# Kernel tuning notes

Measured on AMD Instinct MI355X. Metric: run time of the kernel, lower is better.

The kernel has to match this reference:

```python
import jax, jax.numpy as jnp
import numpy as np

EPS = 1e-8  # torch.nn.CosineSimilarity default eps


def setup_inputs() -> dict:
    key = jax.random.key(0)
    mapping = jax.random.normal(key, (8192, 512), dtype=jnp.float32)
    return {"mapping": mapping}


def reference(mapping) -> jnp.ndarray:
    # Pairwise cosine distance: 1 - (x_i . x_j) / max(||x_i||*||x_j||, eps)
    # Efficient form: single N x D GEMM + outer product of norms
    dots = mapping @ mapping.T                      # [N, N]
    norms = jnp.linalg.norm(mapping, axis=-1)       # [N]
    denom = jnp.maximum(norms[:, None] * norms[None, :], EPS)
    return 1.0 - dots / denom
```

## Files before the change

kernel.cpp:

```cpp
#include <hip/hip_runtime.h>

typedef __attribute__((ext_vector_type(8))) short bf16x8;
typedef __attribute__((ext_vector_type(8))) unsigned short u16x8;
typedef __attribute__((ext_vector_type(4))) float f32x4;

__device__ __forceinline__ unsigned short f2bf(float f) {
    unsigned int u = __float_as_uint(f);
    u += 0x7fffu + ((u >> 16) & 1u);
    return (unsigned short)(u >> 16);
}

__global__ __launch_bounds__(256) void normalize_rows(
    const float* __restrict__ X, unsigned short* __restrict__ Y) {
    const int wave = threadIdx.x >> 6;
    const int lane = threadIdx.x & 63;
    const long row = (long)blockIdx.x * 4 + wave;

    const float4* xr = (const float4*)(X + row * 512);
    float4 a = xr[lane * 2];
    float4 b = xr[lane * 2 + 1];

    float s = a.x * a.x + a.y * a.y + a.z * a.z + a.w * a.w
            + b.x * b.x + b.y * b.y + b.z * b.z + b.w * b.w;
#pragma unroll
    for (int off = 32; off; off >>= 1) s += __shfl_xor(s, off, 64);

    const float inv = rsqrtf(s);

    u16x8 o;
    o[0] = f2bf(a.x * inv); o[1] = f2bf(a.y * inv);
    o[2] = f2bf(a.z * inv); o[3] = f2bf(a.w * inv);
    o[4] = f2bf(b.x * inv); o[5] = f2bf(b.y * inv);
    o[6] = f2bf(b.z * inv); o[7] = f2bf(b.w * inv);
    ((u16x8*)(Y + row * 512))[lane] = o;
}

#define GLDS16(g, l)                                                         \
    __builtin_amdgcn_global_load_lds(                                        \
        (const __attribute__((address_space(1))) void*)(g),                  \
        (__attribute__((address_space(3))) void*)(l), 16, 0, 0)

#define RD(base, r, c) \
    (*(const bf16x8*)((base) + (r) * 64 + ((((c) ^ ((r) & 7))) << 3)))

__global__ __launch_bounds__(512, 2) void cosdist_gemm_sym(
    const unsigned short* __restrict__ Y, float* __restrict__ out) {
    constexpr int N = 8192, K = 512, BM = 256;
    constexpr int NT = N / BM;
    constexpr int A2 = 2 * NT + 1;
    constexpr int TILE = BM * 64;

    __shared__ __align__(16) short As[2 * TILE];
    __shared__ __align__(16) short Bs[2 * TILE];

    constexpr int NWG = NT * (NT + 1) / 2;
    constexpr int CPX = NWG / 8;
    const int hw = blockIdx.x;
    const int p = (hw & 7) * CPX + (hw >> 3);

    int bi = (int)floorf(((float)A2 - sqrtf((float)(A2 * A2) - 8.0f * (float)p)) * 0.5f);
    while ((bi + 1) * (A2 - (bi + 1)) / 2 <= p) ++bi;
    while (bi * (A2 - bi) / 2 > p) --bi;
    const int bj = bi + (p - bi * (A2 - bi) / 2);
    const int bm = bi * BM, bn = bj * BM;

    const int tid  = threadIdx.x;
    const int lane = tid & 63;
    const int wave = tid >> 6;
    const int wr = wave >> 2;
    const int wc = wave & 3;
    const int frow = lane & 15;
    const int fch  = lane >> 4;

    const int srow = tid >> 3;
    const int sgc  = (tid & 7) ^ (srow & 7);
    const unsigned short* Abase = Y + (size_t)(bm + srow) * K + (sgc << 3);
    const unsigned short* Bbase = Y + (size_t)(bn + srow) * K + (sgc << 3);
    const size_t QSTEP = (size_t)64 * K;

    f32x4 acc[8][4] = {};

#pragma unroll
    for (int j = 0; j < 4; ++j) {
        GLDS16(Abase + (size_t)j * QSTEP, As + j * 4096 + tid * 8);
        GLDS16(Bbase + (size_t)j * QSTEP, Bs + j * 4096 + tid * 8);
    }
    __syncthreads();

    for (int kt = 0; kt < 8; ++kt) {
        const short* Ac = As + (kt & 1) * TILE;
        const short* Bc = Bs + (kt & 1) * TILE;
        short* An = As + ((kt + 1) & 1) * TILE;
        short* Bn = Bs + ((kt + 1) & 1) * TILE;
        const int kn = (kt + 1) << 6;
        const bool pf = (kt < 7);

        bf16x8 af[4][2], bfv[2][2];

        if (pf) {
            GLDS16(Abase + kn, An + tid * 8);
            GLDS16(Bbase + kn, Bn + tid * 8);
        }
#pragma unroll
        for (int m = 0; m < 4; ++m) {
            const int r = wr * 128 + m * 16 + frow;
            af[m][0] = RD(Ac, r, fch);
            af[m][1] = RD(Ac, r, 4 + fch);
        }
#pragma unroll
        for (int n = 0; n < 2; ++n) {
            const int r = wc * 64 + n * 16 + frow;
            bfv[n][0] = RD(Bc, r, fch);
            bfv[n][1] = RD(Bc, r, 4 + fch);
        }
        __builtin_amdgcn_s_setprio(1);
#pragma unroll
        for (int m = 0; m < 4; ++m)
#pragma unroll
            for (int n = 0; n < 2; ++n)
#pragma unroll
                for (int kk = 0; kk < 2; ++kk)
                    acc[m][n] = __builtin_amdgcn_mfma_f32_16x16x32_bf16(
                        af[m][kk], bfv[n][kk], acc[m][n], 0, 0, 0);
        __builtin_amdgcn_s_setprio(0);
        __builtin_amdgcn_s_barrier();

        if (pf) {
            GLDS16(Abase + kn + QSTEP, An + 4096 + tid * 8);
            GLDS16(Bbase + kn + QSTEP, Bn + 4096 + tid * 8);
        }
#pragma unroll
        for (int n = 0; n < 2; ++n) {
            const int r = wc * 64 + (n + 2) * 16 + frow;
            bfv[n][0] = RD(Bc, r, fch);
            bfv[n][1] = RD(Bc, r, 4 + fch);
        }
        __builtin_amdgcn_s_setprio(1);
#pragma unroll
        for (int m = 0; m < 4; ++m)
#pragma unroll
            for (int n = 0; n < 2; ++n)
#pragma unroll
                for (int kk = 0; kk < 2; ++kk)
                    acc[m][n + 2] = __builtin_amdgcn_mfma_f32_16x16x32_bf16(
                        af[m][kk], bfv[n][kk], acc[m][n + 2], 0, 0, 0);
        __builtin_amdgcn_s_setprio(0);
        __builtin_amdgcn_s_barrier();

        if (pf) {
            GLDS16(Abase + kn + 2 * QSTEP, An + 2 * 4096 + tid * 8);
            GLDS16(Bbase + kn + 2 * QSTEP, Bn + 2 * 4096 + tid * 8);
        }
#pragma unroll
        for (int m = 0; m < 4; ++m) {
            const int r = wr * 128 + (m + 4) * 16 + frow;
            af[m][0] = RD(Ac, r, fch);
            af[m][1] = RD(Ac, r, 4 + fch);
        }
        __builtin_amdgcn_s_setprio(1);
#pragma unroll
        for (int m = 0; m < 4; ++m)
#pragma unroll
            for (int n = 0; n < 2; ++n)
#pragma unroll
                for (int kk = 0; kk < 2; ++kk)
                    acc[m + 4][n + 2] = __builtin_amdgcn_mfma_f32_16x16x32_bf16(
                        af[m][kk], bfv[n][kk], acc[m + 4][n + 2], 0, 0, 0);
        __builtin_amdgcn_s_setprio(0);
        __builtin_amdgcn_s_barrier();

        if (pf) {
            GLDS16(Abase + kn + 3 * QSTEP, An + 3 * 4096 + tid * 8);
            GLDS16(Bbase + kn + 3 * QSTEP, Bn + 3 * 4096 + tid * 8);
        }
#pragma unroll
        for (int n = 0; n < 2; ++n) {
            const int r = wc * 64 + n * 16 + frow;
            bfv[n][0] = RD(Bc, r, fch);
            bfv[n][1] = RD(Bc, r, 4 + fch);
        }
        __builtin_amdgcn_s_setprio(1);
#pragma unroll
        for (int m = 0; m < 4; ++m)
#pragma unroll
            for (int n = 0; n < 2; ++n)
#pragma unroll
                for (int kk = 0; kk < 2; ++kk)
                    acc[m + 4][n] = __builtin_amdgcn_mfma_f32_16x16x32_bf16(
                        af[m][kk], bfv[n][kk], acc[m + 4][n], 0, 0, 0);
        __builtin_amdgcn_s_setprio(0);
        __syncthreads();
    }

    const int rbase = bm + wr * 128 + (fch << 2);
    const int cbase = bn + wc * 64 + frow;
    const bool offdiag = (bm != bn);

#pragma unroll
    for (int m = 0; m < 8; ++m)
#pragma unroll
        for (int n = 0; n < 4; ++n) {
            f32x4 v;
#pragma unroll
            for (int r = 0; r < 4; ++r) v[r] = 1.0f - acc[m][n][r];
            const int row = rbase + m * 16;
            const int col = cbase + n * 16;

            *(f32x4*)&out[(size_t)col * N + row] = v;

            if (offdiag) {
#pragma unroll
                for (int r = 0; r < 4; ++r)
                    out[(size_t)(row + r) * N + col] = v[r];
            }
        }
}

extern "C" void kernel_launch(void* const* d_in, const int* in_sizes, int n_in,
                              void* d_out, int out_size, void* d_ws, size_t ws_size,
                              hipStream_t stream) {
    const float* X = (const float*)d_in[0];
    float* out = (float*)d_out;
    unsigned short* Y = (unsigned short*)d_ws;

    const int D = 512;
    const int N = in_sizes[0] / D;

    normalize_rows<<<N / 4, 256, 0, stream>>>(X, Y);

    const int nt = N / 256;
    const int ntiles = nt * (nt + 1) / 2;
    cosdist_gemm_sym<<<ntiles, 512, 0, stream>>>(Y, out);
}
```

Baseline: 372.4 us.

## Reorder tile loads by consumption order and use fine-grained vmcnt waits

Reorders the global-to-LDS load slices of A and B so that the quarter needed first by each phase arrives first. It regroups B rows into 32-row halves per 64-row block to match the per-phase fragment reads. The full __syncthreads at the end of each k-step is replaced with partial s_waitcnt vmcnt plus barriers, so the next tile's loads can stay in flight while compute continues. This aims to cut the stall on whole-tile completion. It relies on precise vmcnt counting and barrier placement, which risks LDS races if any count is wrong.

```diff
diff --git a/kernel.cpp b/kernel.cpp
--- a/kernel.cpp
+++ b/kernel.cpp
@@ -72,20 +72,23 @@
     const int frow = lane & 15;
     const int fch  = lane >> 4;
 
-    const int srow = tid >> 3;
-    const int sgc  = (tid & 7) ^ (srow & 7);
-    const unsigned short* Abase = Y + (size_t)(bm + srow) * K + (sgc << 3);
-    const unsigned short* Bbase = Y + (size_t)(bn + srow) * K + (sgc << 3);
-    const size_t QSTEP = (size_t)64 * K;
+    const int i6  = tid >> 3;
+    const int sgc = (tid & 7) ^ (i6 & 7);
+    const unsigned short* Asrc = Y + (size_t)(bm + i6) * K + (sgc << 3);
+    const int rB = ((i6 >> 5) << 6) + (i6 & 31);
+    const unsigned short* Bsrc = Y + (size_t)(bn + rB) * K + (sgc << 3);
+    const int boff = ((i6 >> 5) << 12) + ((i6 & 31) << 6) + ((tid & 7) << 3);
 
     f32x4 acc[8][4] = {};
 
-#pragma unroll
-    for (int j = 0; j < 4; ++j) {
-        GLDS16(Abase + (size_t)j * QSTEP, As + j * 4096 + tid * 8);
-        GLDS16(Bbase + (size_t)j * QSTEP, Bs + j * 4096 + tid * 8);
-    }
-    __syncthreads();
+    GLDS16(Asrc,                   As + tid * 8);
+    GLDS16(Asrc + 2 * 32768,       As + 2 * 4096 + tid * 8);
+    GLDS16(Asrc + 1 * 32768,       As + 1 * 4096 + tid * 8);
+    GLDS16(Asrc + 3 * 32768,       As + 3 * 4096 + tid * 8);
+    GLDS16(Bsrc,                   Bs + boff);
+    GLDS16(Bsrc + 65536,           Bs + 8192 + boff);
+    GLDS16(Bsrc + 16384,           Bs + 2048 + boff);
+    GLDS16(Bsrc + 81920,           Bs + 10240 + boff);
 
     for (int kt = 0; kt < 8; ++kt) {
         const short* Ac = As + (kt & 1) * TILE;
@@ -97,9 +100,11 @@
 
         bf16x8 af[4][2], bfv[2][2];
 
-        if (pf) {
-            GLDS16(Abase + kn, An + tid * 8);
-            GLDS16(Bbase + kn, Bn + tid * 8);
+        asm volatile("s_waitcnt vmcnt(2)" ::: "memory");
+        __builtin_amdgcn_s_barrier();
+        if (pf) {
+            GLDS16(Asrc + kn,             An + tid * 8);
+            GLDS16(Asrc + 2 * 32768 + kn, An + 2 * 4096 + tid * 8);
         }
 #pragma unroll
         for (int m = 0; m < 4; ++m) {
@@ -123,15 +128,17 @@
                     acc[m][n] = __builtin_amdgcn_mfma_f32_16x16x32_bf16(
                         af[m][kk], bfv[n][kk], acc[m][n], 0, 0, 0);
         __builtin_amdgcn_s_setprio(0);
-        __builtin_amdgcn_s_barrier();
-
-        if (pf) {
-            GLDS16(Abase + kn + QSTEP, An + 4096 + tid * 8);
-            GLDS16(Bbase + kn + QSTEP, Bn + 4096 + tid * 8);
+
+        if (pf) asm volatile("s_waitcnt vmcnt(2)" ::: "memory");
+        else    asm volatile("s_waitcnt vmcnt(0)" ::: "memory");
+        __builtin_amdgcn_s_barrier();
+        if (pf) {
+            GLDS16(Asrc + 1 * 32768 + kn, An + 1 * 4096 + tid * 8);
+            GLDS16(Asrc + 3 * 32768 + kn, An + 3 * 4096 + tid * 8);
         }
 #pragma unroll
         for (int n = 0; n < 2; ++n) {
-            const int r = wc * 64 + (n + 2) * 16 + frow;
+            const int r = wc * 64 + 32 + n * 16 + frow;
             bfv[n][0] = RD(Bc, r, fch);
             bfv[n][1] = RD(Bc, r, 4 + fch);
         }
@@ -145,15 +152,15 @@
                     acc[m][n + 2] = __builtin_amdgcn_mfma_f32_16x16x32_bf16(
                         af[m][kk], bfv[n][kk], acc[m][n + 2], 0, 0, 0);
         __builtin_amdgcn_s_setprio(0);
-        __builtin_amdgcn_s_barrier();
-
-        if (pf) {
-            GLDS16(Abase + kn + 2 * QSTEP, An + 2 * 4096 + tid * 8);
-            GLDS16(Bbase + kn + 2 * QSTEP, Bn + 2 * 4096 + tid * 8);
+
+        __builtin_amdgcn_s_barrier();
+        if (pf) {
+            GLDS16(Bsrc + kn,         Bn + boff);
+            GLDS16(Bsrc + 65536 + kn, Bn + 8192 + boff);
         }
 #pragma unroll
         for (int m = 0; m < 4; ++m) {
-            const int r = wr * 128 + (m + 4) * 16 + frow;
+            const int r = wr * 128 + 64 + m * 16 + frow;
             af[m][0] = RD(Ac, r, fch);
             af[m][1] = RD(Ac, r, 4 + fch);
         }
@@ -167,11 +174,11 @@
                     acc[m + 4][n + 2] = __builtin_amdgcn_mfma_f32_16x16x32_bf16(
                         af[m][kk], bfv[n][kk], acc[m + 4][n + 2], 0, 0, 0);
         __builtin_amdgcn_s_setprio(0);
-        __builtin_amdgcn_s_barrier();
-
-        if (pf) {
-            GLDS16(Abase + kn + 3 * QSTEP, An + 3 * 4096 + tid * 8);
-            GLDS16(Bbase + kn + 3 * QSTEP, Bn + 3 * 4096 + tid * 8);
+
+        __builtin_amdgcn_s_barrier();
+        if (pf) {
+            GLDS16(Bsrc + 16384 + kn, Bn + 2048 + boff);
+            GLDS16(Bsrc + 81920 + kn, Bn + 10240 + boff);
         }
 #pragma unroll
         for (int n = 0; n < 2; ++n) {
@@ -189,7 +196,6 @@
                     acc[m + 4][n] = __builtin_amdgcn_mfma_f32_16x16x32_bf16(
                         af[m][kk], bfv[n][kk], acc[m + 4][n], 0, 0, 0);
         __builtin_amdgcn_s_setprio(0);
-        __syncthreads();
     }
 
     const int rbase = bm + wr * 128 + (fch << 2);
```

Result: no change. 369.0 us (-0.9%).
